# Kernel tuning notes

Hardware: AMD Instinct MI355X
Metric: run time of the kernel (lower is better)

## Reference

```python
import jax, jax.numpy as jnp
import numpy as np

NUM_HEADS = 16
MASKED_BIAS = -10000.0


def setup_inputs() -> dict:
    key = jax.random.key(0)
    k1, k2, k3 = jax.random.split(key, 3)
    B, S, D = 2, 2048, 1024
    return {
        "hidden_states": jax.random.normal(k1, (B, S, D), dtype=jnp.float32),
        "c_attn_w": jax.random.normal(k2, (D, 3 * D), dtype=jnp.float32) * 0.02,
        "c_attn_b": jnp.zeros((3 * D,), dtype=jnp.float32),
        "c_proj_w": jax.random.normal(k3, (D, D), dtype=jnp.float32) * 0.02,
        "c_proj_b": jnp.zeros((D,), dtype=jnp.float32),
    }


def reference(hidden_states, c_attn_w, c_attn_b, c_proj_w, c_proj_b):
    B, S, D = hidden_states.shape
    H = NUM_HEADS
    hd = D // H

    qkv = hidden_states @ c_attn_w + c_attn_b  # [B, S, 3D]
    q, k, v = jnp.split(qkv, 3, axis=-1)

    def split_heads(t):
        return t.reshape(B, S, H, hd).transpose(0, 2, 1, 3)  # [B, H, S, hd]

    q, k, v = split_heads(q), split_heads(k), split_heads(v)

    attn_weights = jnp.einsum("bhqd,bhkd->bhqk", q, k)
    attn_weights = attn_weights / jnp.sqrt(jnp.float32(hd))
    # multiplicative causal mask, matching eager GPT2: w*mask + (-1e4)*(1-mask)
    causal = jnp.tril(jnp.ones((S, S), dtype=attn_weights.dtype))  # [S, S]
    attn_weights = attn_weights * causal + MASKED_BIAS * (1.0 - causal)
    attn_weights = jax.nn.softmax(attn_weights, axis=-1)

    attn_output = jnp.einsum("bhqk,bhkd->bhqd", attn_weights, v)
    attn_output = attn_output.transpose(0, 2, 1, 3).reshape(B, S, D)
    attn_output = attn_output @ c_proj_w + c_proj_b
    return attn_output, attn_weights
```

## Files before the change

### kernel.cpp

```cpp
#include <hip/hip_runtime.h>


typedef __bf16 bf16_t;
typedef bf16_t bf16x8 __attribute__((ext_vector_type(8)));
typedef float f32x4 __attribute__((ext_vector_type(4)));
typedef unsigned short ushort8 __attribute__((ext_vector_type(8)));
typedef unsigned short ushort4v __attribute__((ext_vector_type(4)));

#define SEQ 2048
#define DMODEL 1024
#define MTOT 4096

#define AS1 __attribute__((address_space(1)))
#define AS3 __attribute__((address_space(3)))

__device__ __forceinline__ unsigned short f2bf(float f) {
  return __builtin_bit_cast(unsigned short, (bf16_t)f);
}
__device__ __forceinline__ bf16x8 ldb8(const unsigned short* p) {
  return __builtin_bit_cast(bf16x8, *(const ushort8*)p);
}
__device__ __forceinline__ f32x4 mfma16(bf16x8 a, bf16x8 b, f32x4 c) {
  return __builtin_amdgcn_mfma_f32_16x16x32_bf16(a, b, c, 0, 0, 0);
}
__device__ __forceinline__ void gload16(const unsigned short* g, unsigned short* l) {
  __builtin_amdgcn_global_load_lds((AS1 const void*)g, (AS3 void*)l, 16, 0, 0);
}

__global__ __launch_bounds__(256) void cast_kernel(const float* __restrict__ in,
                                                   unsigned short* __restrict__ out) {
  int i = blockIdx.x * 256 + threadIdx.x;
  float4 v = ((const float4*)in)[i];
  ushort4v o;
  o[0] = f2bf(v.x); o[1] = f2bf(v.y); o[2] = f2bf(v.z); o[3] = f2bf(v.w);
  ((ushort4v*)out)[i] = o;
}

__global__ __launch_bounds__(256) void transpose_cast_kernel(const float* __restrict__ in,
                                                             unsigned short* __restrict__ out,
                                                             int R, int C) {
  __shared__ float tile[32][33];
  int c0 = blockIdx.x * 32, r0 = blockIdx.y * 32;
  int tx = threadIdx.x & 31, ty = threadIdx.x >> 5;
#pragma unroll
  for (int i = 0; i < 4; ++i)
    tile[ty + i * 8][tx] = in[(size_t)(r0 + ty + i * 8) * C + c0 + tx];
  __syncthreads();
#pragma unroll
  for (int i = 0; i < 4; ++i)
    out[(size_t)(c0 + ty + i * 8) * R + r0 + tx] = f2bf(tile[tx][ty + i * 8]);
}

template <int EPI>
__global__ __launch_bounds__(256) void gemm128(
    const unsigned short* __restrict__ A, const unsigned short* __restrict__ BT,
    const float* __restrict__ bias, float* __restrict__ outF,
    unsigned short* __restrict__ qws, unsigned short* __restrict__ kws,
    unsigned short* __restrict__ vws, int M, int N, int K) {
  __shared__ unsigned short Alds[128 * 32];
  __shared__ unsigned short Blds[128 * 32];
  int m0 = blockIdx.x * 128, n0 = blockIdx.y * 128;
  int t = threadIdx.x;
  int l = t & 63, j = l & 15, g = l >> 4;
  int w = t >> 6, wr = w >> 1, wc = w & 1;

  f32x4 acc[4][4];
#pragma unroll
  for (int mi = 0; mi < 4; ++mi)
#pragma unroll
    for (int st = 0; st < 4; ++st)
#pragma unroll
      for (int r = 0; r < 4; ++r) acc[mi][st][r] = 0.f;

  int srow = t >> 2;
  int scol = (t & 3) * 8;
  const unsigned short* aB0 = A + (size_t)(m0 + srow) * K + scol;
  const unsigned short* aB1 = aB0 + (size_t)64 * K;
  const unsigned short* bB0 = BT + (size_t)(n0 + srow) * K + scol;
  const unsigned short* bB1 = bB0 + (size_t)64 * K;
  unsigned short* aL0 = &Alds[srow * 32 + scol];
  unsigned short* aL1 = aL0 + 64 * 32;
  unsigned short* bL0 = &Blds[srow * 32 + scol];
  unsigned short* bL1 = bL0 + 64 * 32;

  for (int k0 = 0; k0 < K; k0 += 32) {
    __syncthreads();
    gload16(aB0 + k0, aL0);
    gload16(aB1 + k0, aL1);
    gload16(bB0 + k0, bL0);
    gload16(bB1 + k0, bL1);
    __syncthreads();
    bf16x8 af[4], bfr[4];
#pragma unroll
    for (int mi = 0; mi < 4; ++mi) af[mi] = ldb8(&Alds[(wr * 64 + mi * 16 + j) * 32 + g * 8]);
#pragma unroll
    for (int st = 0; st < 4; ++st) bfr[st] = ldb8(&Blds[(wc * 64 + st * 16 + j) * 32 + g * 8]);
#pragma unroll
    for (int mi = 0; mi < 4; ++mi)
#pragma unroll
      for (int st = 0; st < 4; ++st) acc[mi][st] = mfma16(af[mi], bfr[st], acc[mi][st]);
  }

#pragma unroll
  for (int st = 0; st < 4; ++st) {
    int n = n0 + wc * 64 + st * 16 + j;
    float bv = bias[n];
#pragma unroll
    for (int mi = 0; mi < 4; ++mi)
#pragma unroll
      for (int r = 0; r < 4; ++r) {
        int m = m0 + wr * 64 + mi * 16 + g * 4 + r;
        float val = acc[mi][st][r] + bv;
        if (EPI == 1) {
          outF[(size_t)m * N + n] = val;
        } else {
          int region = n >> 10;
          int h = (n & 1023) >> 6;
          int d = n & 63;
          int bb = m >> 11, s = m & 2047;
          int bh = bb * 16 + h;
          if (region == 0) qws[(((size_t)bh) * SEQ + s) * 64 + d] = f2bf(val * 0.125f);
          else if (region == 1) kws[(((size_t)bh) * SEQ + s) * 64 + d] = f2bf(val);
          else vws[(((size_t)bh) * 64 + d) * SEQ + s] = f2bf(val);
        }
      }
  }
}

__global__ __launch_bounds__(256) void attn_flash(
    const unsigned short* __restrict__ qg, const unsigned short* __restrict__ kg,
    const unsigned short* __restrict__ vg, float* __restrict__ linvb,
    unsigned short* __restrict__ ointer) {
  __shared__ unsigned short Klds[64][72];
  __shared__ unsigned short Vlds[64][72];
  __shared__ unsigned short Plds[4][16 * 72];

  int qt = 31 - blockIdx.x;
  int bh = blockIdx.y;
  int b = bh >> 4, h = bh & 15;
  int t = threadIdx.x;
  int w = t >> 6, l = t & 63, j = l & 15, g = l >> 4;

  const unsigned short* qb = qg + (size_t)bh * SEQ * 64;
  const unsigned short* kb = kg + (size_t)bh * SEQ * 64;
  const unsigned short* vb = vg + (size_t)bh * SEQ * 64;

  int qr_a = qt * 64 + w * 16 + j;
  bf16x8 qa0 = ldb8(&qb[(size_t)qr_a * 64 + g * 8]);
  bf16x8 qa1 = ldb8(&qb[(size_t)qr_a * 64 + 32 + g * 8]);

  int qrow0 = qt * 64 + w * 16 + g * 4;

  int skey = t >> 2;
  int sc = (t & 3) * 8;

  float lpart[4] = {0.f, 0.f, 0.f, 0.f};
  f32x4 oacc[4];
#pragma unroll
  for (int st = 0; st < 4; ++st)
#pragma unroll
    for (int r = 0; r < 4; ++r) oacc[st][r] = 0.f;

  for (int kt = 0; kt <= qt; ++kt) {
    __syncthreads();
    {
      const unsigned short* src = &kb[(size_t)(kt * 64 + skey) * 64];
      *(ushort8*)&Klds[skey][sc] = *(const ushort8*)&src[sc];
      *(ushort8*)&Klds[skey][sc + 32] = *(const ushort8*)&src[sc + 32];
      const unsigned short* vsrc = &vb[(size_t)skey * SEQ + kt * 64];
      *(ushort8*)&Vlds[skey][sc] = *(const ushort8*)&vsrc[sc];
      *(ushort8*)&Vlds[skey][sc + 32] = *(const ushort8*)&vsrc[sc + 32];
    }
    __syncthreads();
    f32x4 sacc[4];
#pragma unroll
    for (int st = 0; st < 4; ++st)
#pragma unroll
      for (int r = 0; r < 4; ++r) sacc[st][r] = 0.f;
#pragma unroll
    for (int st = 0; st < 4; ++st) {
      bf16x8 kf0 = ldb8(&Klds[st * 16 + j][g * 8]);
      bf16x8 kf1 = ldb8(&Klds[st * 16 + j][32 + g * 8]);
      sacc[st] = mfma16(qa0, kf0, sacc[st]);
      sacc[st] = mfma16(qa1, kf1, sacc[st]);
    }
    bool diag = (kt == qt);
#pragma unroll
    for (int st = 0; st < 4; ++st)
#pragma unroll
      for (int r = 0; r < 4; ++r) {
        float p = __expf(sacc[st][r]);
        if (diag) {
          int kc = kt * 64 + st * 16 + j;
          p = (kc > qrow0 + r) ? 0.f : p;
        }
        lpart[r] += p;
        Plds[w][(g * 4 + r) * 72 + st * 16 + j] = f2bf(p);
      }
    bf16x8 pa0 = ldb8(&Plds[w][j * 72 + g * 8]);
    bf16x8 pa1 = ldb8(&Plds[w][j * 72 + 32 + g * 8]);
#pragma unroll
    for (int st = 0; st < 4; ++st) {
      bf16x8 vf0 = ldb8(&Vlds[st * 16 + j][g * 8]);
      bf16x8 vf1 = ldb8(&Vlds[st * 16 + j][32 + g * 8]);
      oacc[st] = mfma16(pa0, vf0, oacc[st]);
      oacc[st] = mfma16(pa1, vf1, oacc[st]);
    }
  }

  float linv[4];
#pragma unroll
  for (int r = 0; r < 4; ++r) {
    float sum = lpart[r];
#pragma unroll
    for (int o = 1; o < 16; o <<= 1) sum += __shfl_xor(sum, o);
    linv[r] = 1.f / sum;
  }
  if (j == 0) {
#pragma unroll
    for (int r = 0; r < 4; ++r) linvb[(size_t)bh * SEQ + qrow0 + r] = linv[r];
  }
#pragma unroll
  for (int st = 0; st < 4; ++st)
#pragma unroll
    for (int r = 0; r < 4; ++r) {
      int qrow = qrow0 + r;
      int d = st * 16 + j;
      ointer[((size_t)b * SEQ + qrow) * DMODEL + h * 64 + d] = f2bf(oacc[st][r] * linv[r]);
    }
}

__global__ __launch_bounds__(256) void pwrite_kernel(
    const unsigned short* __restrict__ qg, const unsigned short* __restrict__ kg,
    const float* __restrict__ linvb, float* __restrict__ outw) {
  int kj = blockIdx.x, qi = blockIdx.y, bh = blockIdx.z;
  float* outrow = outw + (size_t)bh * SEQ * SEQ;
  int t = threadIdx.x;

  if (kj > qi) {
    int row = qi * 128 + (t >> 1);
    float4* dst = (float4*)&outrow[(size_t)row * SEQ + kj * 128 + (t & 1) * 64];
    float4 z = make_float4(0.f, 0.f, 0.f, 0.f);
#pragma unroll
    for (int i = 0; i < 16; ++i) dst[i] = z;
    return;
  }

  __shared__ unsigned short Qlds[128 * 72];
  __shared__ unsigned short Klds[128 * 72];
  int l = t & 63, j = l & 15, g = l >> 4;
  int w = t >> 6, wr = w >> 1, wc = w & 1;

  {
    int srow = t >> 1;
    int cb = (t & 1) * 32;
    const unsigned short* qsrc = qg + ((size_t)bh * SEQ + qi * 128 + srow) * 64 + cb;
    const unsigned short* ksrc = kg + ((size_t)bh * SEQ + kj * 128 + srow) * 64 + cb;
#pragma unroll
    for (int i = 0; i < 4; ++i) {
      *(ushort8*)&Qlds[srow * 72 + cb + i * 8] = *(const ushort8*)&qsrc[i * 8];
      *(ushort8*)&Klds[srow * 72 + cb + i * 8] = *(const ushort8*)&ksrc[i * 8];
    }
  }
  __syncthreads();

  f32x4 acc[4][4];
#pragma unroll
  for (int mi = 0; mi < 4; ++mi)
#pragma unroll
    for (int st = 0; st < 4; ++st)
#pragma unroll
      for (int r = 0; r < 4; ++r) acc[mi][st][r] = 0.f;

#pragma unroll
  for (int kk = 0; kk < 2; ++kk) {
    bf16x8 af[4], bfr[4];
#pragma unroll
    for (int mi = 0; mi < 4; ++mi)
      af[mi] = ldb8(&Qlds[(wr * 64 + mi * 16 + j) * 72 + kk * 32 + g * 8]);
#pragma unroll
    for (int st = 0; st < 4; ++st)
      bfr[st] = ldb8(&Klds[(wc * 64 + st * 16 + j) * 72 + kk * 32 + g * 8]);
#pragma unroll
    for (int mi = 0; mi < 4; ++mi)
#pragma unroll
      for (int st = 0; st < 4; ++st) acc[mi][st] = mfma16(af[mi], bfr[st], acc[mi][st]);
  }

#pragma unroll
  for (int mi = 0; mi < 4; ++mi)
#pragma unroll
    for (int r = 0; r < 4; ++r) {
      int qrow = qi * 128 + wr * 64 + mi * 16 + g * 4 + r;
      float lv = linvb[(size_t)bh * SEQ + qrow];
      float* orow = &outrow[(size_t)qrow * SEQ];
#pragma unroll
      for (int st = 0; st < 4; ++st) {
        int kc = kj * 128 + wc * 64 + st * 16 + j;
        float p = (kc > qrow) ? 0.f : __expf(acc[mi][st][r]) * lv;
        orow[kc] = p;
      }
    }
}

extern "C" void kernel_launch(void* const* d_in, const int* in_sizes, int n_in,
                              void* d_out, int out_size, void* d_ws, size_t ws_size,
                              hipStream_t stream) {
  const float* hidden = (const float*)d_in[0];
  const float* w_attn = (const float*)d_in[1];
  const float* b_attn = (const float*)d_in[2];
  const float* w_proj = (const float*)d_in[3];
  const float* b_proj = (const float*)d_in[4];

  float* out_attn = (float*)d_out;
  float* out_w = out_attn + (size_t)MTOT * DMODEL;

  char* ws = (char*)d_ws;
  unsigned short* hbf = (unsigned short*)(ws);
  unsigned short* w1T = (unsigned short*)(ws + 8388608);
  unsigned short* w2T = (unsigned short*)(ws + 14680064);
  unsigned short* qws = (unsigned short*)(ws + 16777216);
  unsigned short* kws = (unsigned short*)(ws + 25165824);
  unsigned short* vws = (unsigned short*)(ws + 33554432);
  float* linvb = (float*)(ws + 8388608);

  cast_kernel<<<4096, 256, 0, stream>>>(hidden, hbf);
  transpose_cast_kernel<<<dim3(96, 32), 256, 0, stream>>>(w_attn, w1T, 1024, 3072);
  transpose_cast_kernel<<<dim3(32, 32), 256, 0, stream>>>(w_proj, w2T, 1024, 1024);
  gemm128<0><<<dim3(32, 24), 256, 0, stream>>>(hbf, w1T, b_attn, nullptr, qws, kws, vws,
                                               MTOT, 3 * DMODEL, DMODEL);
  attn_flash<<<dim3(32, 32), 256, 0, stream>>>(qws, kws, vws, linvb, hbf);
  pwrite_kernel<<<dim3(16, 16, 32), 256, 0, stream>>>(qws, kws, linvb, out_w);
  gemm128<1><<<dim3(32, 8), 256, 0, stream>>>(hbf, w2T, b_proj, out_attn, nullptr, nullptr,
                                              nullptr, MTOT, DMODEL, DMODEL);
}
```

Before: 304.3 us.

## Load K and V MFMA fragments directly from global memory, dropping LDS staging

After: 449.3 us. 47.6% more time.

```diff
diff --git a/kernel.cpp b/kernel.cpp
--- a/kernel.cpp
+++ b/kernel.cpp
@@ -131,8 +131,6 @@
     const unsigned short* __restrict__ qg, const unsigned short* __restrict__ kg,
     const unsigned short* __restrict__ vg, float* __restrict__ linvb,
     unsigned short* __restrict__ ointer) {
-  __shared__ unsigned short Klds[64][72];
-  __shared__ unsigned short Vlds[64][72];
   __shared__ unsigned short Plds[4][16 * 72];
 
   int qt = 31 - blockIdx.x;
@@ -151,8 +149,9 @@
 
   int qrow0 = qt * 64 + w * 16 + g * 4;
 
-  int skey = t >> 2;
-  int sc = (t & 3) * 8;
+  const unsigned short* kfb = kb + (size_t)j * 64 + g * 8;
+  const unsigned short* vfb = vb + (size_t)j * SEQ + g * 8;
+  unsigned short* Pw = &Plds[w][0];
 
   float lpart[4] = {0.f, 0.f, 0.f, 0.f};
   f32x4 oacc[4];
@@ -162,16 +161,13 @@
     for (int r = 0; r < 4; ++r) oacc[st][r] = 0.f;
 
   for (int kt = 0; kt <= qt; ++kt) {
-    __syncthreads();
-    {
-      const unsigned short* src = &kb[(size_t)(kt * 64 + skey) * 64];
-      *(ushort8*)&Klds[skey][sc] = *(const ushort8*)&src[sc];
-      *(ushort8*)&Klds[skey][sc + 32] = *(const ushort8*)&src[sc + 32];
-      const unsigned short* vsrc = &vb[(size_t)skey * SEQ + kt * 64];
-      *(ushort8*)&Vlds[skey][sc] = *(const ushort8*)&vsrc[sc];
-      *(ushort8*)&Vlds[skey][sc + 32] = *(const ushort8*)&vsrc[sc + 32];
-    }
-    __syncthreads();
+    const unsigned short* ktk = kfb + (size_t)kt * 64 * 64;
+    bf16x8 kf0[4], kf1[4];
+#pragma unroll
+    for (int st = 0; st < 4; ++st) {
+      kf0[st] = ldb8(ktk + st * 16 * 64);
+      kf1[st] = ldb8(ktk + st * 16 * 64 + 32);
+    }
     f32x4 sacc[4];
 #pragma unroll
     for (int st = 0; st < 4; ++st)
@@ -179,10 +175,8 @@
       for (int r = 0; r < 4; ++r) sacc[st][r] = 0.f;
 #pragma unroll
     for (int st = 0; st < 4; ++st) {
-      bf16x8 kf0 = ldb8(&Klds[st * 16 + j][g * 8]);
-      bf16x8 kf1 = ldb8(&Klds[st * 16 + j][32 + g * 8]);
-      sacc[st] = mfma16(qa0, kf0, sacc[st]);
-      sacc[st] = mfma16(qa1, kf1, sacc[st]);
+      sacc[st] = mfma16(qa0, kf0[st], sacc[st]);
+      sacc[st] = mfma16(qa1, kf1[st], sacc[st]);
     }
     bool diag = (kt == qt);
 #pragma unroll
@@ -195,14 +189,15 @@
           p = (kc > qrow0 + r) ? 0.f : p;
         }
         lpart[r] += p;
-        Plds[w][(g * 4 + r) * 72 + st * 16 + j] = f2bf(p);
+        Pw[(g * 4 + r) * 72 + st * 16 + j] = f2bf(p);
       }
-    bf16x8 pa0 = ldb8(&Plds[w][j * 72 + g * 8]);
-    bf16x8 pa1 = ldb8(&Plds[w][j * 72 + 32 + g * 8]);
+    bf16x8 pa0 = ldb8(&Pw[j * 72 + g * 8]);
+    bf16x8 pa1 = ldb8(&Pw[j * 72 + 32 + g * 8]);
+    const unsigned short* ktv = vfb + kt * 64;
 #pragma unroll
     for (int st = 0; st < 4; ++st) {
-      bf16x8 vf0 = ldb8(&Vlds[st * 16 + j][g * 8]);
-      bf16x8 vf1 = ldb8(&Vlds[st * 16 + j][32 + g * 8]);
+      bf16x8 vf0 = ldb8(ktv + (size_t)st * 16 * SEQ);
+      bf16x8 vf1 = ldb8(ktv + (size_t)st * 16 * SEQ + 32);
       oacc[st] = mfma16(pa0, vf0, oacc[st]);
       oacc[st] = mfma16(pa1, vf1, oacc[st]);
     }
```
